# Kernel tuning notes

Hardware: AMD Instinct MI355X
Metric: run time of the kernel (lower is better)

## Reference

```python
import jax, jax.numpy as jnp
import numpy as np

COMMITMENT_COST = 0.25


def setup_inputs() -> dict:
    key = jax.random.key(0)
    k1, k2 = jax.random.split(key)
    inputs = jax.random.normal(k1, (32, 64, 64, 64), dtype=jnp.float32)  # b c h w
    num_embeddings, embedding_dim = 1024, 64
    # matches torch uniform_(-1/K, 1/K) init distributionally
    embedding = jax.random.uniform(
        k2, (num_embeddings, embedding_dim), dtype=jnp.float32,
        minval=-1.0 / num_embeddings, maxval=1.0 / num_embeddings)
    return {"inputs": inputs, "embedding": embedding}


def reference(inputs, embedding):
    # b c h w -> b h w c
    x = jnp.transpose(inputs, (0, 2, 3, 1))
    b, h, w, c = x.shape
    flat = x.reshape(-1, c)  # [N, D]
    dists = (jnp.sum(flat * flat, axis=1, keepdims=True)
             + jnp.sum(embedding * embedding, axis=1)
             - 2.0 * flat @ embedding.T)  # [N, K]
    idx = jnp.argmin(dists, axis=1)  # [N]
    quantized = embedding[idx].reshape(b, h, w, c)  # gather == one-hot matmul
    # elementwise MSE losses (reduction='none'); stop-gradient mirrors .detach()
    e_latent = (jax.lax.stop_gradient(quantized) - x) ** 2
    q_latent = (quantized - jax.lax.stop_gradient(x)) ** 2
    loss = q_latent + COMMITMENT_COST * e_latent  # [b, h, w, c]
    # straight-through estimator
    quantized_st = x + jax.lax.stop_gradient(quantized - x)
    quantized_out = jnp.transpose(quantized_st, (0, 3, 1, 2))  # b h w c -> b c h w
    return quantized_out, loss, idx.reshape(b, h, w)
```

## Files before the change

### kernel.cpp

```cpp
#include <hip/hip_runtime.h>

#define NPTS    131072
#define KC      1024
#define DD      64
#define HWSZ    4096
#define MARGINF 6e-5f

typedef __attribute__((ext_vector_type(8))) short short8;
typedef __attribute__((ext_vector_type(4))) float f32x4;

__device__ __forceinline__ ushort bf16_rne(float x) {
    unsigned u = __float_as_uint(x);
    unsigned r = u + 0x7fffu + ((u >> 16) & 1u);
    return (ushort)(r >> 16);
}

__global__ void __launch_bounds__(256)
vq_prep_e(const float* __restrict__ emb, float* __restrict__ se32,
          float* __restrict__ sebB, ushort* __restrict__ Ebuf,
          float* __restrict__ embT, int* __restrict__ cnt) {
    __shared__ float es[16][68];
    const int tid  = threadIdx.x;
    const int tile = blockIdx.x;
    const int kbase = tile * 16;

    if (tile == 0 && tid == 0) *cnt = 0;

#pragma unroll
    for (int it = 0; it < 4; ++it) {
        int f = it * 256 + tid;
        es[f >> 6][f & 63] = emb[(size_t)kbase * DD + f];
    }
    __syncthreads();

    if (tid < 16) {
        float rr[8];
#pragma unroll
        for (int di = 0; di < 8; ++di) rr[di] = 0.0f;
        {
#pragma clang fp contract(off)
#pragma unroll
            for (int dm = 0; dm < 8; ++dm)
#pragma unroll
                for (int di = 0; di < 8; ++di) {
                    float ev = es[tid][dm * 8 + di];
                    rr[di] += ev * ev;
                }
        }
        float s;
        {
#pragma clang fp contract(off)
            s = ((rr[0] + rr[1]) + (rr[2] + rr[3])) + ((rr[4] + rr[5]) + (rr[6] + rr[7]));
        }
        se32[kbase + tid] = s;
        sebB[kbase + tid] = s + 0.5f;
    }

#pragma unroll
    for (int it = 0; it < 4; ++it) {
        int f = it * 256 + tid;
        int d = f >> 4, colk = f & 15;
        embT[d * KC + kbase + colk] = es[colk][d];
    }

#pragma unroll
    for (int it = 0; it < 8; ++it) {
        int f = it * 256 + tid;
        int sub = f >> 9;
        int pos = f & 511;
        int kh = sub >> 1, hl = sub & 1;
        int jj = pos & 7, colk = (pos >> 3) & 15, quad = pos >> 7;
        float ev = es[colk][kh * 32 + quad * 8 + jj];
        ushort hb = bf16_rne(ev);
        ushort val;
        if (hl == 0) {
            val = hb;
        } else {
            float hf = __uint_as_float(((unsigned)hb) << 16);
            val = bf16_rne(ev - hf);
        }
        Ebuf[((tile * 2 + kh) * 2 + hl) * 512 + pos] = val;
    }
}

__global__ void __launch_bounds__(256)
vq_main(const float* __restrict__ in, const float* __restrict__ emb,
        const ushort* __restrict__ Ebuf, const float* __restrict__ sebB,
        float* __restrict__ outq, float* __restrict__ outl, float* __restrict__ outi,
        int* __restrict__ cnt, int* __restrict__ queue) {
    __shared__ float xs[64][129];
    __shared__ int   sidx[128];
    const int tid = threadIdx.x;
    const int n0  = blockIdx.x * 128;
    const int b   = n0 >> 12;
    const int hw0 = n0 & 4095;
    const float* inb = in + (size_t)b * DD * HWSZ;

#pragma unroll
    for (int it = 0; it < 32; ++it) {
        int f = tid + it * 256;
        int c = f >> 7, j = f & 127;
        xs[c][j] = inb[c * HWSZ + hw0 + j];
    }
    __syncthreads();

    const int lane = tid & 63, wave = tid >> 6;
    const int quad = lane >> 4, col = lane & 15;

    short8 A[2][2][2];
#pragma unroll
    for (int p = 0; p < 2; ++p) {
        int pt = wave * 32 + p * 16 + col;
#pragma unroll
        for (int kh = 0; kh < 2; ++kh) {
            short8 ah, al;
#pragma unroll
            for (int j = 0; j < 8; ++j) {
                float xv = xs[kh * 32 + quad * 8 + j][pt];
                ushort hb = bf16_rne(xv);
                float  hf = __uint_as_float(((unsigned)hb) << 16);
                ah[j] = (short)hb;
                al[j] = (short)bf16_rne(xv - hf);
            }
            A[p][kh][0] = ah; A[p][kh][1] = al;
        }
    }

    unsigned b1[8], b2[8];
#pragma unroll
    for (int s = 0; s < 8; ++s) { b1[s] = 0xFFFFFFFFu; b2[s] = 0xFFFFFFFFu; }

    for (int g = 0; g < 16; ++g) {
        short8 B[4][2][2];
        float  sB[4];
#pragma unroll
        for (int s = 0; s < 4; ++s) {
            int tile = g * 4 + s;
            sB[s] = sebB[tile * 16 + col];
#pragma unroll
            for (int kh = 0; kh < 2; ++kh)
#pragma unroll
                for (int hl = 0; hl < 2; ++hl)
                    B[s][kh][hl] = *(const short8*)(Ebuf + ((tile * 2 + kh) * 2 + hl) * 512 + lane * 8);
        }
        f32x4 acc[2][4];
#pragma unroll
        for (int p = 0; p < 2; ++p)
#pragma unroll
            for (int s = 0; s < 4; ++s) acc[p][s] = (f32x4){0.f, 0.f, 0.f, 0.f};
#pragma unroll
        for (int p = 0; p < 2; ++p)
#pragma unroll
            for (int s = 0; s < 4; ++s) {
                acc[p][s] = __builtin_amdgcn_mfma_f32_16x16x32_bf16(A[p][0][0], B[s][0][0], acc[p][s], 0, 0, 0);
                acc[p][s] = __builtin_amdgcn_mfma_f32_16x16x32_bf16(A[p][1][0], B[s][1][0], acc[p][s], 0, 0, 0);
                acc[p][s] = __builtin_amdgcn_mfma_f32_16x16x32_bf16(A[p][0][0], B[s][0][1], acc[p][s], 0, 0, 0);
                acc[p][s] = __builtin_amdgcn_mfma_f32_16x16x32_bf16(A[p][1][0], B[s][1][1], acc[p][s], 0, 0, 0);
                acc[p][s] = __builtin_amdgcn_mfma_f32_16x16x32_bf16(A[p][0][1], B[s][0][0], acc[p][s], 0, 0, 0);
                acc[p][s] = __builtin_amdgcn_mfma_f32_16x16x32_bf16(A[p][1][1], B[s][1][0], acc[p][s], 0, 0, 0);
            }
#pragma unroll
        for (int p = 0; p < 2; ++p)
#pragma unroll
            for (int r = 0; r < 4; ++r) {
                unsigned q[4];
#pragma unroll
                for (int s = 0; s < 4; ++s) {
                    float t = fmaf(-2.f, acc[p][s][r], sB[s]);
                    q[s] = (__float_as_uint(t) & 0xFFFFFFC0u) | (unsigned)(g * 4 + s);
                }
                unsigned a  = min(q[0], q[1]), bb = max(q[0], q[1]);
                unsigned c2 = min(q[2], q[3]), d2 = max(q[2], q[3]);
                unsigned lo = min(a, c2), hi = max(a, c2);
                unsigned sec = min(min(bb, d2), hi);
                int sl = p * 4 + r;
                b2[sl] = min(min(b2[sl], sec), max(b1[sl], lo));
                b1[sl] = min(b1[sl], lo);
            }
    }

    unsigned v1[8], v2[8]; int ci[8];
#pragma unroll
    for (int s = 0; s < 8; ++s) {
        ci[s] = (int)(b1[s] & 63u) * 16 + col;
        v1[s] = b1[s] & 0xFFFFFFC0u;
        v2[s] = b2[s] & 0xFFFFFFC0u;
    }
#pragma unroll
    for (int off = 1; off < 16; off <<= 1) {
#pragma unroll
        for (int s = 0; s < 8; ++s) {
            unsigned o1 = (unsigned)__shfl_xor((int)v1[s], off);
            unsigned o2 = (unsigned)__shfl_xor((int)v2[s], off);
            int      oi = __shfl_xor(ci[s], off);
            unsigned nb2 = min(min(v2[s], o2), max(v1[s], o1));
            bool take = (o1 < v1[s]) || (o1 == v1[s] && oi < ci[s]);
            v1[s] = take ? o1 : v1[s];
            ci[s] = take ? oi : ci[s];
            v2[s] = nb2;
        }
    }
#pragma unroll
    for (int s = 0; s < 8; ++s) {
        if (col == s) {
            int jloc = wave * 32 + (s >> 2) * 16 + quad * 4 + (s & 3);
            sidx[jloc] = ci[s];
            float f1 = __uint_as_float(v1[s]), f2 = __uint_as_float(v2[s]);
            if (f2 - f1 < MARGINF) { int pos = atomicAdd(cnt, 1); queue[pos] = n0 + jloc; }
        }
    }
    __syncthreads();

    for (int t = 0; t < 32; ++t) {
        int jloc = wave * 32 + t;
        int kidx = sidx[jloc];
        float qv = emb[kidx * DD + lane];
        float x  = xs[lane][jloc];
        float dv = qv - x;
        float l  = dv * dv;
        outl[(size_t)(n0 + jloc) * DD + lane] = fmaf(0.25f, l, l);
        outq[((size_t)(b * DD) + lane) * HWSZ + hw0 + jloc] = x + (qv - x);
    }
    if (lane < 32) outi[n0 + wave * 32 + lane] = (float)sidx[wave * 32 + lane];
}

__global__ void __launch_bounds__(256)
vq_fix(const float* __restrict__ in, const float* __restrict__ emb,
       const float* __restrict__ embT, const float* __restrict__ se32,
       const int* __restrict__ queue, const int* __restrict__ cnt,
       float* __restrict__ outq, float* __restrict__ outl, float* __restrict__ outi) {
    const int lane = threadIdx.x & 63;
    const int gw   = blockIdx.x * 4 + (threadIdx.x >> 6);
    const int nwav = gridDim.x * 4;
    const int total = *cnt;
    for (int q0 = gw * 4; q0 < total; q0 += nwav * 4) {
        int   nn[4]; bool vld[4];
        float xr[4], sx4[4];
#pragma unroll
        for (int i = 0; i < 4; ++i) {
            int qi = q0 + i;
            vld[i] = (qi < total);
            nn[i]  = queue[vld[i] ? qi : q0];
            int b = nn[i] >> 12, hw = nn[i] & 4095;
            xr[i] = in[(size_t)b * DD * HWSZ + (size_t)lane * HWSZ + hw];
        }
#pragma unroll
        for (int i = 0; i < 4; ++i) {
            float rr[8];
#pragma unroll
            for (int di = 0; di < 8; ++di) rr[di] = 0.0f;
            for (int dm = 0; dm < 8; ++dm) {
#pragma unroll
                for (int di = 0; di < 8; ++di) {
                    float xv = __int_as_float(
                        __builtin_amdgcn_readlane(__float_as_int(xr[i]), dm * 8 + di));
                    {
#pragma clang fp contract(off)
                        rr[di] += xv * xv;
                    }
                }
            }
            {
#pragma clang fp contract(off)
                sx4[i] = ((rr[0] + rr[1]) + (rr[2] + rr[3])) + ((rr[4] + rr[5]) + (rr[6] + rr[7]));
            }
        }

        float bD[4]; int bi[4];
#pragma unroll
        for (int i = 0; i < 4; ++i) { bD[i] = 3.4e38f; bi[i] = 0x7fffffff; }

        for (int pass = 0; pass < 4; ++pass) {
            double acc[16];
#pragma unroll
            for (int a = 0; a < 16; ++a) acc[a] = 0.0;
            const float* rpb = embT + (lane << 4) + pass * 4;
            for (int dm = 0; dm < 8; ++dm) {
#pragma unroll
                for (int di = 0; di < 8; ++di) {
                    const int d = dm * 8 + di;
                    f32x4 ev = *(const f32x4*)(rpb + (size_t)d * KC);
                    double xd0 = (double)__int_as_float(
                        __builtin_amdgcn_readlane(__float_as_int(xr[0]), d));
                    double xd1 = (double)__int_as_float(
                        __builtin_amdgcn_readlane(__float_as_int(xr[1]), d));
                    double xd2 = (double)__int_as_float(
                        __builtin_amdgcn_readlane(__float_as_int(xr[2]), d));
                    double xd3 = (double)__int_as_float(
                        __builtin_amdgcn_readlane(__float_as_int(xr[3]), d));
#pragma unroll
                    for (int j = 0; j < 4; ++j) {
                        double e = (double)ev[j];
                        acc[0 * 4 + j] = fma(xd0, e, acc[0 * 4 + j]);
                        acc[1 * 4 + j] = fma(xd1, e, acc[1 * 4 + j]);
                        acc[2 * 4 + j] = fma(xd2, e, acc[2 * 4 + j]);
                        acc[3 * 4 + j] = fma(xd3, e, acc[3 * 4 + j]);
                    }
                }
            }
#pragma unroll
            for (int j = 0; j < 4; ++j) {
                int k = (lane << 4) + pass * 4 + j;
                float sek = se32[k];
#pragma unroll
                for (int i = 0; i < 4; ++i) {
                    float m2 = (float)(2.0 * acc[i * 4 + j]);
                    float s1, Dv;
                    {
#pragma clang fp contract(off)
                        s1 = sx4[i] + sek;
                        Dv = s1 - m2;
                    }
                    if (Dv < bD[i]) { bD[i] = Dv; bi[i] = k; }
                }
            }
        }

#pragma unroll
        for (int i = 0; i < 4; ++i) {
            float d = bD[i]; int ix = bi[i];
#pragma unroll
            for (int off = 32; off > 0; off >>= 1) {
                float oD = __shfl_down(d, off);
                int   oi = __shfl_down(ix, off);
                if (oD < d || (oD == d && oi < ix)) { d = oD; ix = oi; }
            }
            ix = __shfl(ix, 0);
            if (vld[i]) {
                int n = nn[i];
                int old = (int)outi[n];
                if (ix != old) {
                    int bb = n >> 12, hw = n & 4095;
                    float xv = xr[i];
                    float qv = emb[ix * DD + lane];
                    float dv = qv - xv;
                    float l  = dv * dv;
                    outl[(size_t)n * DD + lane] = fmaf(0.25f, l, l);
                    outq[((size_t)bb * DD + lane) * HWSZ + hw] = xv + (qv - xv);
                    if (lane == 0) outi[n] = (float)ix;
                }
            }
        }
    }
}

extern "C" void kernel_launch(void* const* d_in, const int* in_sizes, int n_in,
                              void* d_out, int out_size, void* d_ws, size_t ws_size,
                              hipStream_t stream) {
    const float* in  = (const float*)d_in[0];
    const float* emb = (const float*)d_in[1];

    float* outq = (float*)d_out;
    float* outl = outq + (size_t)NPTS * DD;
    float* outi = outl + (size_t)NPTS * DD;

    char*   ws    = (char*)d_ws;
    float*  se32  = (float*)ws;
    float*  sebB  = (float*)(ws + 4096);
    ushort* Ebuf  = (ushort*)(ws + 8192);
    float*  embT  = (float*)(ws + 8192 + 262144);
    int*    cnt   = (int*)(ws + 8192 + 262144 + 262144);
    int*    queue = (int*)(ws + 8192 + 262144 + 262144 + 256);

    vq_prep_e<<<64, 256, 0, stream>>>(emb, se32, sebB, Ebuf, embT, cnt);
    vq_main<<<NPTS / 128, 256, 0, stream>>>(in, emb, Ebuf, sebB, outq, outl, outi, cnt, queue);
    vq_fix<<<1024, 256, 0, stream>>>(in, emb, embT, se32, queue, cnt, outq, outl, outi);
}
```

Baseline: 226.1 us.

## Fuse ambiguous-point refinement into main kernel with fp32 prefilter and fp64 recheck

Removes the separate vq_fix kernel and its global atomic queue. Each vq_main block now collects its ambiguous points in shared memory and rescans them itself. The rescan computes all 1024 distances in fp32, then recomputes in fp64 only the candidates within a slack of the minimum. This removes a kernel launch, the global atomic contention and the reload of inputs, and cuts fp64 work to a few candidates. In exchange, vq_main has a serial tail in blocks that hold many ambiguous points, and the fp32 prefilter slack has to be wide enough to keep the correct argmin.

```diff
diff --git a/kernel.cpp b/kernel.cpp
--- a/kernel.cpp
+++ b/kernel.cpp
@@ -5,6 +5,7 @@
 #define DD      64
 #define HWSZ    4096
 #define MARGINF 6e-5f
+#define SLACKF  3e-5f
 
 typedef __attribute__((ext_vector_type(8))) short short8;
 typedef __attribute__((ext_vector_type(4))) float f32x4;
@@ -18,13 +19,11 @@
 __global__ void __launch_bounds__(256)
 vq_prep_e(const float* __restrict__ emb, float* __restrict__ se32,
           float* __restrict__ sebB, ushort* __restrict__ Ebuf,
-          float* __restrict__ embT, int* __restrict__ cnt) {
+          float* __restrict__ embT) {
     __shared__ float es[16][68];
     const int tid  = threadIdx.x;
     const int tile = blockIdx.x;
     const int kbase = tile * 16;
-
-    if (tile == 0 && tid == 0) *cnt = 0;
 
 #pragma unroll
     for (int it = 0; it < 4; ++it) {
@@ -86,15 +85,19 @@
 __global__ void __launch_bounds__(256)
 vq_main(const float* __restrict__ in, const float* __restrict__ emb,
         const ushort* __restrict__ Ebuf, const float* __restrict__ sebB,
-        float* __restrict__ outq, float* __restrict__ outl, float* __restrict__ outi,
-        int* __restrict__ cnt, int* __restrict__ queue) {
+        const float* __restrict__ se32, const float* __restrict__ embT,
+        float* __restrict__ outq, float* __restrict__ outl, float* __restrict__ outi) {
     __shared__ float xs[64][129];
     __shared__ int   sidx[128];
+    __shared__ int   ambCnt;
+    __shared__ int   ambList[128];
     const int tid = threadIdx.x;
     const int n0  = blockIdx.x * 128;
     const int b   = n0 >> 12;
     const int hw0 = n0 & 4095;
     const float* inb = in + (size_t)b * DD * HWSZ;
+
+    if (tid == 0) ambCnt = 0;
 
 #pragma unroll
     for (int it = 0; it < 32; ++it) {
@@ -206,7 +209,7 @@
             int jloc = wave * 32 + (s >> 2) * 16 + quad * 4 + (s & 3);
             sidx[jloc] = ci[s];
             float f1 = __uint_as_float(v1[s]), f2 = __uint_as_float(v2[s]);
-            if (f2 - f1 < MARGINF) { int pos = atomicAdd(cnt, 1); queue[pos] = n0 + jloc; }
+            if (f2 - f1 < MARGINF) { int p = atomicAdd(&ambCnt, 1); ambList[p] = jloc; }
         }
     }
     __syncthreads();
@@ -222,124 +225,101 @@
         outq[((size_t)(b * DD) + lane) * HWSZ + hw0 + jloc] = x + (qv - x);
     }
     if (lane < 32) outi[n0 + wave * 32 + lane] = (float)sidx[wave * 32 + lane];
-}
-
-__global__ void __launch_bounds__(256)
-vq_fix(const float* __restrict__ in, const float* __restrict__ emb,
-       const float* __restrict__ embT, const float* __restrict__ se32,
-       const int* __restrict__ queue, const int* __restrict__ cnt,
-       float* __restrict__ outq, float* __restrict__ outl, float* __restrict__ outi) {
-    const int lane = threadIdx.x & 63;
-    const int gw   = blockIdx.x * 4 + (threadIdx.x >> 6);
-    const int nwav = gridDim.x * 4;
-    const int total = *cnt;
-    for (int q0 = gw * 4; q0 < total; q0 += nwav * 4) {
-        int   nn[4]; bool vld[4];
-        float xr[4], sx4[4];
-#pragma unroll
-        for (int i = 0; i < 4; ++i) {
-            int qi = q0 + i;
-            vld[i] = (qi < total);
-            nn[i]  = queue[vld[i] ? qi : q0];
-            int b = nn[i] >> 12, hw = nn[i] & 4095;
-            xr[i] = in[(size_t)b * DD * HWSZ + (size_t)lane * HWSZ + hw];
-        }
-#pragma unroll
-        for (int i = 0; i < 4; ++i) {
-            float rr[8];
-#pragma unroll
-            for (int di = 0; di < 8; ++di) rr[di] = 0.0f;
-            for (int dm = 0; dm < 8; ++dm) {
-#pragma unroll
-                for (int di = 0; di < 8; ++di) {
-                    float xv = __int_as_float(
-                        __builtin_amdgcn_readlane(__float_as_int(xr[i]), dm * 8 + di));
-                    {
-#pragma clang fp contract(off)
-                        rr[di] += xv * xv;
-                    }
-                }
-            }
-            {
-#pragma clang fp contract(off)
-                sx4[i] = ((rr[0] + rr[1]) + (rr[2] + rr[3])) + ((rr[4] + rr[5]) + (rr[6] + rr[7]));
-            }
-        }
-
-        float bD[4]; int bi[4];
-#pragma unroll
-        for (int i = 0; i < 4; ++i) { bD[i] = 3.4e38f; bi[i] = 0x7fffffff; }
-
-        for (int pass = 0; pass < 4; ++pass) {
-            double acc[16];
-#pragma unroll
-            for (int a = 0; a < 16; ++a) acc[a] = 0.0;
-            const float* rpb = embT + (lane << 4) + pass * 4;
-            for (int dm = 0; dm < 8; ++dm) {
-#pragma unroll
-                for (int di = 0; di < 8; ++di) {
-                    const int d = dm * 8 + di;
-                    f32x4 ev = *(const f32x4*)(rpb + (size_t)d * KC);
-                    double xd0 = (double)__int_as_float(
-                        __builtin_amdgcn_readlane(__float_as_int(xr[0]), d));
-                    double xd1 = (double)__int_as_float(
-                        __builtin_amdgcn_readlane(__float_as_int(xr[1]), d));
-                    double xd2 = (double)__int_as_float(
-                        __builtin_amdgcn_readlane(__float_as_int(xr[2]), d));
-                    double xd3 = (double)__int_as_float(
-                        __builtin_amdgcn_readlane(__float_as_int(xr[3]), d));
-#pragma unroll
-                    for (int j = 0; j < 4; ++j) {
-                        double e = (double)ev[j];
-                        acc[0 * 4 + j] = fma(xd0, e, acc[0 * 4 + j]);
-                        acc[1 * 4 + j] = fma(xd1, e, acc[1 * 4 + j]);
-                        acc[2 * 4 + j] = fma(xd2, e, acc[2 * 4 + j]);
-                        acc[3 * 4 + j] = fma(xd3, e, acc[3 * 4 + j]);
-                    }
-                }
-            }
-#pragma unroll
-            for (int j = 0; j < 4; ++j) {
-                int k = (lane << 4) + pass * 4 + j;
-                float sek = se32[k];
-#pragma unroll
-                for (int i = 0; i < 4; ++i) {
-                    float m2 = (float)(2.0 * acc[i * 4 + j]);
-                    float s1, Dv;
-                    {
-#pragma clang fp contract(off)
-                        s1 = sx4[i] + sek;
-                        Dv = s1 - m2;
-                    }
-                    if (Dv < bD[i]) { bD[i] = Dv; bi[i] = k; }
-                }
-            }
-        }
-
-#pragma unroll
-        for (int i = 0; i < 4; ++i) {
-            float d = bD[i]; int ix = bi[i];
-#pragma unroll
-            for (int off = 32; off > 0; off >>= 1) {
-                float oD = __shfl_down(d, off);
-                int   oi = __shfl_down(ix, off);
-                if (oD < d || (oD == d && oi < ix)) { d = oD; ix = oi; }
-            }
-            ix = __shfl(ix, 0);
-            if (vld[i]) {
-                int n = nn[i];
-                int old = (int)outi[n];
-                if (ix != old) {
-                    int bb = n >> 12, hw = n & 4095;
-                    float xv = xr[i];
-                    float qv = emb[ix * DD + lane];
-                    float dv = qv - xv;
-                    float l  = dv * dv;
-                    outl[(size_t)n * DD + lane] = fmaf(0.25f, l, l);
-                    outq[((size_t)bb * DD + lane) * HWSZ + hw] = xv + (qv - xv);
-                    if (lane == 0) outi[n] = (float)ix;
-                }
-            }
+    __syncthreads();
+
+    const int namb = ambCnt;
+    for (int a = wave; a < namb; a += 4) {
+        const int jloc = ambList[a];
+        float rr[8];
+#pragma unroll
+        for (int di = 0; di < 8; ++di) rr[di] = 0.0f;
+        for (int dm = 0; dm < 8; ++dm) {
+#pragma unroll
+            for (int di = 0; di < 8; ++di) {
+                float xv = xs[dm * 8 + di][jloc];
+                {
+#pragma clang fp contract(off)
+                    rr[di] += xv * xv;
+                }
+            }
+        }
+        float sx;
+        {
+#pragma clang fp contract(off)
+            sx = ((rr[0] + rr[1]) + (rr[2] + rr[3])) + ((rr[4] + rr[5]) + (rr[6] + rr[7]));
+        }
+
+        float af[16];
+#pragma unroll
+        for (int c = 0; c < 16; ++c) af[c] = 0.0f;
+        const float* rpb = embT + (lane << 4);
+        for (int dm = 0; dm < 8; ++dm) {
+#pragma unroll
+            for (int di = 0; di < 8; ++di) {
+                const int d = dm * 8 + di;
+                const float* rp = rpb + (size_t)d * KC;
+                f32x4 e0 = *(const f32x4*)(rp + 0);
+                f32x4 e1 = *(const f32x4*)(rp + 4);
+                f32x4 e2 = *(const f32x4*)(rp + 8);
+                f32x4 e3 = *(const f32x4*)(rp + 12);
+                float xv = xs[d][jloc];
+#pragma unroll
+                for (int c = 0; c < 4; ++c) {
+                    af[c + 0]  = fmaf(xv, e0[c], af[c + 0]);
+                    af[c + 4]  = fmaf(xv, e1[c], af[c + 4]);
+                    af[c + 8]  = fmaf(xv, e2[c], af[c + 8]);
+                    af[c + 12] = fmaf(xv, e3[c], af[c + 12]);
+                }
+            }
+        }
+#pragma unroll
+        for (int c = 0; c < 16; ++c) {
+            float s1 = sx + se32[(lane << 4) + c];
+            af[c] = s1 - 2.0f * af[c];
+        }
+        float fm = af[0];
+#pragma unroll
+        for (int c = 1; c < 16; ++c) fm = fminf(fm, af[c]);
+#pragma unroll
+        for (int off = 1; off < 64; off <<= 1)
+            fm = fminf(fm, __shfl_xor(fm, off));
+        const float thr = fm + SLACKF;
+
+        float bDe = 3.4e38f; int bie = 0x7fffffff;
+#pragma unroll
+        for (int c = 0; c < 16; ++c) {
+            if (af[c] < thr) {
+                const int k = (lane << 4) + c;
+                const float* er = emb + k * DD;
+                double acc = 0.0;
+#pragma unroll
+                for (int d = 0; d < DD; ++d)
+                    acc = fma((double)xs[d][jloc], (double)er[d], acc);
+                float m2 = (float)(2.0 * acc);
+                float s1, Dv;
+                {
+#pragma clang fp contract(off)
+                    s1 = sx + se32[k];
+                    Dv = s1 - m2;
+                }
+                if (Dv < bDe) { bDe = Dv; bie = k; }
+            }
+        }
+#pragma unroll
+        for (int off = 32; off > 0; off >>= 1) {
+            float oD = __shfl_down(bDe, off);
+            int   oi = __shfl_down(bie, off);
+            if (oD < bDe || (oD == bDe && oi < bie)) { bDe = oD; bie = oi; }
+        }
+        bie = __shfl(bie, 0);
+        if (bie != sidx[jloc]) {
+            float qv = emb[bie * DD + lane];
+            float x  = xs[lane][jloc];
+            float dv = qv - x;
+            float l  = dv * dv;
+            outl[(size_t)(n0 + jloc) * DD + lane] = fmaf(0.25f, l, l);
+            outq[((size_t)(b * DD) + lane) * HWSZ + hw0 + jloc] = x + (qv - x);
+            if (lane == 0) outi[n0 + jloc] = (float)bie;
         }
     }
 }
@@ -359,10 +339,8 @@
     float*  sebB  = (float*)(ws + 4096);
     ushort* Ebuf  = (ushort*)(ws + 8192);
     float*  embT  = (float*)(ws + 8192 + 262144);
-    int*    cnt   = (int*)(ws + 8192 + 262144 + 262144);
-    int*    queue = (int*)(ws + 8192 + 262144 + 262144 + 256);
-
-    vq_prep_e<<<64, 256, 0, stream>>>(emb, se32, sebB, Ebuf, embT, cnt);
-    vq_main<<<NPTS / 128, 256, 0, stream>>>(in, emb, Ebuf, sebB, outq, outl, outi, cnt, queue);
-    vq_fix<<<1024, 256, 0, stream>>>(in, emb, embT, se32, queue, cnt, outq, outl, outi);
+
+    vq_prep_e<<<64, 256, 0, stream>>>(emb, se32, sebB, Ebuf, embT);
+    vq_main<<<NPTS / 128, 256, 0, stream>>>(in, emb, Ebuf, sebB, se32, embT,
+                                            outq, outl, outi);
 }
```

New measurement: 587.0 us. 2.6x slower.

## Screen fix-pass candidates in fp32 and refine only near-ties in double

Applied to the files above, without the earlier changes.

The fix kernel, which re-evaluates queued points flagged as ambiguous, now computes all 1024 distances in fp32 instead of fp64. Each lane tracks its best and second-best value, and fp64 recomputation runs only for codes within a slack of the wave-wide minimum. Each wave now handles 8 points per iteration instead of 4. This is meant to cut the costly double-precision FMA work, but it adds divergent refinement branches, and a slack that is too small could change the selected index in rare near-ties.

```diff
diff --git a/kernel.cpp b/kernel.cpp
--- a/kernel.cpp
+++ b/kernel.cpp
@@ -5,6 +5,7 @@
 #define DD      64
 #define HWSZ    4096
 #define MARGINF 6e-5f
+#define SLACKF  4e-5f
 
 typedef __attribute__((ext_vector_type(8))) short short8;
 typedef __attribute__((ext_vector_type(4))) float f32x4;
@@ -13,6 +14,10 @@
     unsigned u = __float_as_uint(x);
     unsigned r = u + 0x7fffu + ((u >> 16) & 1u);
     return (ushort)(r >> 16);
+}
+
+__device__ __forceinline__ float rdlane(float v, int d) {
+    return __int_as_float(__builtin_amdgcn_readlane(__float_as_int(v), d));
 }
 
 __global__ void __launch_bounds__(256)
@@ -233,11 +238,11 @@
     const int gw   = blockIdx.x * 4 + (threadIdx.x >> 6);
     const int nwav = gridDim.x * 4;
     const int total = *cnt;
-    for (int q0 = gw * 4; q0 < total; q0 += nwav * 4) {
-        int   nn[4]; bool vld[4];
-        float xr[4], sx4[4];
-#pragma unroll
-        for (int i = 0; i < 4; ++i) {
+    for (int q0 = gw * 8; q0 < total; q0 += nwav * 8) {
+        int   nn[8]; bool vld[8];
+        float xr[8], sx8[8];
+#pragma unroll
+        for (int i = 0; i < 8; ++i) {
             int qi = q0 + i;
             vld[i] = (qi < total);
             nn[i]  = queue[vld[i] ? qi : q0];
@@ -245,15 +250,14 @@
             xr[i] = in[(size_t)b * DD * HWSZ + (size_t)lane * HWSZ + hw];
         }
 #pragma unroll
-        for (int i = 0; i < 4; ++i) {
+        for (int i = 0; i < 8; ++i) {
             float rr[8];
 #pragma unroll
             for (int di = 0; di < 8; ++di) rr[di] = 0.0f;
             for (int dm = 0; dm < 8; ++dm) {
 #pragma unroll
                 for (int di = 0; di < 8; ++di) {
-                    float xv = __int_as_float(
-                        __builtin_amdgcn_readlane(__float_as_int(xr[i]), dm * 8 + di));
+                    float xv = rdlane(xr[i], dm * 8 + di);
                     {
 #pragma clang fp contract(off)
                         rr[di] += xv * xv;
@@ -262,39 +266,31 @@
             }
             {
 #pragma clang fp contract(off)
-                sx4[i] = ((rr[0] + rr[1]) + (rr[2] + rr[3])) + ((rr[4] + rr[5]) + (rr[6] + rr[7]));
-            }
-        }
-
-        float bD[4]; int bi[4];
-#pragma unroll
-        for (int i = 0; i < 4; ++i) { bD[i] = 3.4e38f; bi[i] = 0x7fffffff; }
+                sx8[i] = ((rr[0] + rr[1]) + (rr[2] + rr[3])) + ((rr[4] + rr[5]) + (rr[6] + rr[7]));
+            }
+        }
+
+        float m1[8], m2[8]; int i1[8];
+#pragma unroll
+        for (int i = 0; i < 8; ++i) { m1[i] = 3.4e38f; m2[i] = 3.4e38f; i1[i] = 0x7fffffff; }
 
         for (int pass = 0; pass < 4; ++pass) {
-            double acc[16];
-#pragma unroll
-            for (int a = 0; a < 16; ++a) acc[a] = 0.0;
+            float acc[32];
+#pragma unroll
+            for (int a = 0; a < 32; ++a) acc[a] = 0.0f;
             const float* rpb = embT + (lane << 4) + pass * 4;
             for (int dm = 0; dm < 8; ++dm) {
 #pragma unroll
                 for (int di = 0; di < 8; ++di) {
                     const int d = dm * 8 + di;
                     f32x4 ev = *(const f32x4*)(rpb + (size_t)d * KC);
-                    double xd0 = (double)__int_as_float(
-                        __builtin_amdgcn_readlane(__float_as_int(xr[0]), d));
-                    double xd1 = (double)__int_as_float(
-                        __builtin_amdgcn_readlane(__float_as_int(xr[1]), d));
-                    double xd2 = (double)__int_as_float(
-                        __builtin_amdgcn_readlane(__float_as_int(xr[2]), d));
-                    double xd3 = (double)__int_as_float(
-                        __builtin_amdgcn_readlane(__float_as_int(xr[3]), d));
-#pragma unroll
-                    for (int j = 0; j < 4; ++j) {
-                        double e = (double)ev[j];
-                        acc[0 * 4 + j] = fma(xd0, e, acc[0 * 4 + j]);
-                        acc[1 * 4 + j] = fma(xd1, e, acc[1 * 4 + j]);
-                        acc[2 * 4 + j] = fma(xd2, e, acc[2 * 4 + j]);
-                        acc[3 * 4 + j] = fma(xd3, e, acc[3 * 4 + j]);
+#pragma unroll
+                    for (int i = 0; i < 8; ++i) {
+                        float xv = rdlane(xr[i], d);
+                        acc[i * 4 + 0] = fmaf(xv, ev[0], acc[i * 4 + 0]);
+                        acc[i * 4 + 1] = fmaf(xv, ev[1], acc[i * 4 + 1]);
+                        acc[i * 4 + 2] = fmaf(xv, ev[2], acc[i * 4 + 2]);
+                        acc[i * 4 + 3] = fmaf(xv, ev[3], acc[i * 4 + 3]);
                     }
                 }
             }
@@ -303,41 +299,76 @@
                 int k = (lane << 4) + pass * 4 + j;
                 float sek = se32[k];
 #pragma unroll
-                for (int i = 0; i < 4; ++i) {
-                    float m2 = (float)(2.0 * acc[i * 4 + j]);
+                for (int i = 0; i < 8; ++i) {
+                    float s = (sx8[i] + sek) - 2.0f * acc[i * 4 + j];
+                    if (s < m1[i]) { m2[i] = m1[i]; m1[i] = s; i1[i] = k; }
+                    else if (s < m2[i]) m2[i] = s;
+                }
+            }
+        }
+
+#pragma unroll
+        for (int i = 0; i < 8; ++i) {
+            float gm = m1[i];
+#pragma unroll
+            for (int off = 1; off < 64; off <<= 1)
+                gm = fminf(gm, __shfl_xor(gm, off));
+            const float thr = gm + SLACKF;
+
+            float bDe = 3.4e38f; int bie = 0x7fffffff;
+            if (m2[i] <= thr) {
+#pragma unroll 1
+                for (int c = 0; c < 16; ++c) {
+                    const int k = (lane << 4) + c;
+                    const float* er = emb + k * DD;
+                    double acc = 0.0;
+#pragma unroll 4
+                    for (int d = 0; d < DD; ++d)
+                        acc = fma((double)rdlane(xr[i], d), (double)er[d], acc);
+                    float mm = (float)(2.0 * acc);
                     float s1, Dv;
                     {
 #pragma clang fp contract(off)
-                        s1 = sx4[i] + sek;
-                        Dv = s1 - m2;
+                        s1 = sx8[i] + se32[k];
+                        Dv = s1 - mm;
                     }
-                    if (Dv < bD[i]) { bD[i] = Dv; bi[i] = k; }
-                }
-            }
-        }
-
-#pragma unroll
-        for (int i = 0; i < 4; ++i) {
-            float d = bD[i]; int ix = bi[i];
+                    if (Dv < bDe) { bDe = Dv; bie = k; }
+                }
+            } else if (m1[i] <= thr) {
+                const int k = i1[i];
+                const float* er = emb + k * DD;
+                double acc = 0.0;
+#pragma unroll 4
+                for (int d = 0; d < DD; ++d)
+                    acc = fma((double)rdlane(xr[i], d), (double)er[d], acc);
+                float mm = (float)(2.0 * acc);
+                float s1, Dv;
+                {
+#pragma clang fp contract(off)
+                    s1 = sx8[i] + se32[k];
+                    Dv = s1 - mm;
+                }
+                bDe = Dv; bie = k;
+            }
 #pragma unroll
             for (int off = 32; off > 0; off >>= 1) {
-                float oD = __shfl_down(d, off);
-                int   oi = __shfl_down(ix, off);
-                if (oD < d || (oD == d && oi < ix)) { d = oD; ix = oi; }
-            }
-            ix = __shfl(ix, 0);
+                float oD = __shfl_down(bDe, off);
+                int   oi = __shfl_down(bie, off);
+                if (oD < bDe || (oD == bDe && oi < bie)) { bDe = oD; bie = oi; }
+            }
+            bie = __shfl(bie, 0);
             if (vld[i]) {
                 int n = nn[i];
                 int old = (int)outi[n];
-                if (ix != old) {
+                if (bie != old) {
                     int bb = n >> 12, hw = n & 4095;
                     float xv = xr[i];
-                    float qv = emb[ix * DD + lane];
+                    float qv = emb[bie * DD + lane];
                     float dv = qv - xv;
                     float l  = dv * dv;
                     outl[(size_t)n * DD + lane] = fmaf(0.25f, l, l);
                     outq[((size_t)bb * DD + lane) * HWSZ + hw] = xv + (qv - xv);
-                    if (lane == 0) outi[n] = (float)ix;
+                    if (lane == 0) outi[n] = (float)bie;
                 }
             }
         }
```

Measured after the change: 266.3 us. 17.8% more time.
